# Kernel optimization log

Hardware: AMD Instinct MI355X
Metric: run time of the kernel (lower is better)

The kernel has to match this reference:

```python
import jax, jax.numpy as jnp
import numpy as np

H = 128  # hidden_dim
F = 64   # node_feat_dim


def setup_inputs() -> dict:
    key = jax.random.key(0)
    ks = jax.random.split(key, 24)
    N, E, NR, NT = 50000, 400000, 20000, 20000
    inp = {
        "mol_x": jax.random.normal(ks[0], (N, F), jnp.float32),
        "pos": jax.random.normal(ks[1], (N, 3), jnp.float32),
        "reaction_x": jax.random.normal(ks[2], (NR, F), jnp.float32),
        "target_x": jax.random.normal(ks[3], (NT, F), jnp.float32),
        "edge_index": jax.random.randint(ks[4], (2, E), 0, N, jnp.int32),
    }
    def lin(k, fan_in, fan_out):
        s = 1.0 / np.sqrt(fan_in)
        kw, kb = jax.random.split(k)
        W = jax.random.uniform(kw, (fan_in, fan_out), jnp.float32, -s, s)
        b = jax.random.uniform(kb, (fan_out,), jnp.float32, -s, s)
        return W, b
    inp["W_node"], inp["b_node"] = lin(ks[5], F, H)
    inp["W_att1"], inp["b_att1"] = lin(ks[6], 2 * H + 3, H)
    inp["W_att2"], inp["b_att2"] = lin(ks[7], H, 1)
    inp["W_upd"], inp["b_upd"] = lin(ks[8], H, H)
    inp["Wy1"], inp["by1"] = lin(ks[9], H, 64)
    inp["Wy2"], inp["by2"] = lin(ks[10], 64, 1)
    inp["Wa1"], inp["ba1"] = lin(ks[11], H, 64)
    inp["Wa2"], inp["ba2"] = lin(ks[12], 64, 1)
    return inp


def reference(mol_x, pos, reaction_x, target_x, edge_index,
              W_node, b_node, W_att1, b_att1, W_att2, b_att2,
              W_upd, b_upd, Wy1, by1, Wy2, by2, Wa1, ba1, Wa2, ba2):
    N = mol_x.shape[0]
    # node encoder
    h = mol_x @ W_node + b_node                      # [N, H]
    src, dst = edge_index[0], edge_index[1]          # PyG: x_j = source, x_i = target
    x_j = h[src]                                      # [E, H]
    x_i = h[dst]                                      # [E, H]
    dist = pos[dst] - pos[src]                        # [E, 3]
    cat = jnp.concatenate([x_i, x_j, dist], axis=1)   # [E, 2H+3]
    s = jax.nn.relu(cat @ W_att1 + b_att1) @ W_att2 + b_att2  # [E, 1]
    att = jax.nn.softmax(s, axis=0)                   # global softmax over edges (dim=0)
    msg = x_j * att                                   # [E, H]
    aggr = jax.ops.segment_sum(msg, dst, num_segments=N)  # scatter-add -> [N, H]
    mol_feats = aggr @ W_upd + b_upd                  # [N, H]
    # heads on reaction / target graphs
    rh = reaction_x @ W_node + b_node
    th = target_x @ W_node + b_node
    pred_yield = (jax.nn.relu(rh @ Wy1 + by1) @ Wy2 + by2).squeeze(-1)
    pred_activity = (jax.nn.relu(th @ Wa1 + ba1) @ Wa2 + ba2).squeeze(-1)
    return pred_yield, pred_activity, mol_feats
```

## Files before the change

### kernel.cpp

```cpp
#include <hip/hip_runtime.h>
#include <hip/hip_bf16.h>

typedef unsigned short ushort_t;
typedef __attribute__((ext_vector_type(8))) short s16x8;
typedef __attribute__((ext_vector_type(4))) float f32x4;

__device__ inline unsigned short f2bf(float x) {
    unsigned u = __float_as_uint(x);
    return (unsigned short)((u + 0x7FFFu + ((u >> 16) & 1u)) >> 16);
}
__device__ inline float bflo(unsigned u) { return __uint_as_float(u << 16); }
__device__ inline float bfhi(unsigned u) { return __uint_as_float(u & 0xffff0000u); }

__device__ inline void pack_one(const float* __restrict__ W, int K, int N,
                                ushort_t* __restrict__ dst, int g) {
    int KT = K / 32;
    int nt = g / (KT * 64);
    int rem = g % (KT * 64);
    int kt = rem / 64, lane = rem % 64;
    int n = nt * 16 + (lane & 15);
    int kbase = kt * 32 + ((lane >> 4) << 3);
    ushort_t tmp[8];
#pragma unroll
    for (int j = 0; j < 8; ++j) tmp[j] = f2bf(W[(size_t)(kbase + j) * N + n]);
    uint4 pk;
    pk.x = tmp[0] | ((unsigned)tmp[1] << 16);
    pk.y = tmp[2] | ((unsigned)tmp[3] << 16);
    pk.z = tmp[4] | ((unsigned)tmp[5] << 16);
    pk.w = tmp[6] | ((unsigned)tmp[7] << 16);
    *(uint4*)&dst[(size_t)g * 8] = pk;
}

__global__ void convert_w(const float* __restrict__ Wn, const float* __restrict__ W1,
                          const float* __restrict__ Wu, const float* __restrict__ Wy1,
                          const float* __restrict__ Wa1,
                          ushort_t* __restrict__ Wnb, ushort_t* __restrict__ W1tb,
                          ushort_t* __restrict__ W1mb, ushort_t* __restrict__ Wub,
                          ushort_t* __restrict__ Wy1b, ushort_t* __restrict__ Wa1b) {
    int t = blockIdx.x * 256 + threadIdx.x;
    if (t < 1024)       pack_one(Wn, 64, 128, Wnb, t);
    else if (t < 3072)  pack_one(W1, 128, 128, W1tb, t - 1024);
    else if (t < 5120)  pack_one(W1 + 128 * 128, 128, 128, W1mb, t - 3072);
    else if (t < 7168)  pack_one(Wu, 128, 128, Wub, t - 5120);
    else if (t < 8192)  pack_one(Wy1, 128, 64, Wy1b, t - 7168);
    else if (t < 9216)  pack_one(Wa1, 128, 64, Wa1b, t - 8192);
}

__global__ void encode_pq(const float* __restrict__ x, const ushort_t* __restrict__ Wnb,
                          const float* __restrict__ bn, const ushort_t* __restrict__ W1tb,
                          const ushort_t* __restrict__ W1mb, const float* __restrict__ b1,
                          ushort_t* __restrict__ hb, ushort_t* __restrict__ P,
                          ushort_t* __restrict__ Q, int nrows) {
    __shared__ ushort_t ldsX[16 * 72];
    __shared__ ushort_t ldsH[16 * 136];
    int t = threadIdx.x;
    int r0 = blockIdx.x * 16;
    {
        int row = t >> 4, c4 = (t & 15) * 4;
        float4 v = *(const float4*)&x[(size_t)(r0 + row) * 64 + c4];
        uint2 pk;
        pk.x = f2bf(v.x) | ((unsigned)f2bf(v.y) << 16);
        pk.y = f2bf(v.z) | ((unsigned)f2bf(v.w) << 16);
        *(uint2*)&ldsX[row * 72 + c4] = pk;
    }
    __syncthreads();
    int w = t >> 6, lane = t & 63;
    int c = lane & 15, q = lane >> 4;
    int ntA = w, ntB = w + 4;
    {
        f32x4 acc0 = {0.f, 0.f, 0.f, 0.f}, acc1 = acc0;
#pragma unroll
        for (int kt = 0; kt < 2; ++kt) {
            s16x8 a = *(const s16x8*)&ldsX[c * 72 + kt * 32 + q * 8];
            s16x8 b0 = *(const s16x8*)&Wnb[((ntA * 2 + kt) * 64 + lane) * 8];
            s16x8 b1v = *(const s16x8*)&Wnb[((ntB * 2 + kt) * 64 + lane) * 8];
            acc0 = __builtin_amdgcn_mfma_f32_16x16x32_bf16(a, b0, acc0, 0, 0, 0);
            acc1 = __builtin_amdgcn_mfma_f32_16x16x32_bf16(a, b1v, acc1, 0, 0, 0);
        }
        float bi0 = bn[ntA * 16 + c], bi1 = bn[ntB * 16 + c];
#pragma unroll
        for (int r = 0; r < 4; ++r) {
            int row = r0 + q * 4 + r;
            ushort_t h0 = f2bf(acc0[r] + bi0), h1 = f2bf(acc1[r] + bi1);
            ldsH[(q * 4 + r) * 136 + ntA * 16 + c] = h0;
            ldsH[(q * 4 + r) * 136 + ntB * 16 + c] = h1;
            if (row < nrows) {
                hb[(size_t)row * 128 + ntA * 16 + c] = h0;
                hb[(size_t)row * 128 + ntB * 16 + c] = h1;
            }
        }
    }
    __syncthreads();
    {
        f32x4 p0 = {0.f, 0.f, 0.f, 0.f}, p1 = p0, q0 = p0, q1 = p0;
#pragma unroll
        for (int kt = 0; kt < 4; ++kt) {
            s16x8 a = *(const s16x8*)&ldsH[c * 136 + kt * 32 + q * 8];
            s16x8 bp0 = *(const s16x8*)&W1tb[((ntA * 4 + kt) * 64 + lane) * 8];
            s16x8 bp1 = *(const s16x8*)&W1tb[((ntB * 4 + kt) * 64 + lane) * 8];
            s16x8 bq0 = *(const s16x8*)&W1mb[((ntA * 4 + kt) * 64 + lane) * 8];
            s16x8 bq1 = *(const s16x8*)&W1mb[((ntB * 4 + kt) * 64 + lane) * 8];
            p0 = __builtin_amdgcn_mfma_f32_16x16x32_bf16(a, bp0, p0, 0, 0, 0);
            p1 = __builtin_amdgcn_mfma_f32_16x16x32_bf16(a, bp1, p1, 0, 0, 0);
            q0 = __builtin_amdgcn_mfma_f32_16x16x32_bf16(a, bq0, q0, 0, 0, 0);
            q1 = __builtin_amdgcn_mfma_f32_16x16x32_bf16(a, bq1, q1, 0, 0, 0);
        }
        float bi0 = b1[ntA * 16 + c], bi1 = b1[ntB * 16 + c];
#pragma unroll
        for (int r = 0; r < 4; ++r) {
            int row = r0 + q * 4 + r;
            if (row < nrows) {
                P[(size_t)row * 128 + ntA * 16 + c] = f2bf(p0[r] + bi0);
                P[(size_t)row * 128 + ntB * 16 + c] = f2bf(p1[r] + bi1);
                Q[(size_t)row * 128 + ntA * 16 + c] = f2bf(q0[r]);
                Q[(size_t)row * 128 + ntB * 16 + c] = f2bf(q1[r]);
            }
        }
    }
}

__global__ void edge_score(const ushort_t* __restrict__ P, const ushort_t* __restrict__ Q,
                           const float* __restrict__ pos, const int* __restrict__ src,
                           const int* __restrict__ dst, const float* __restrict__ W1b,
                           const float* __restrict__ W2, const float* __restrict__ b2,
                           float* __restrict__ s_out, int* __restrict__ counts,
                           float* __restrict__ redm, float* __restrict__ rede, int E) {
    __shared__ float wsh[4 * 128];
    __shared__ float smm[256], sme[256];
    int t = threadIdx.x;
    for (int i = t; i < 384; i += 256) wsh[i] = W1b[i];
    if (t < 128) wsh[384 + t] = W2[t];
    __syncthreads();
    int w = t >> 6, lane = t & 63;
    int g = lane >> 4;
    int c = lane & 15;
    float w0[8], w1[8], w2[8], wv[8];
#pragma unroll
    for (int j = 0; j < 8; ++j) {
        w0[j] = wsh[c * 8 + j];
        w1[j] = wsh[128 + c * 8 + j];
        w2[j] = wsh[256 + c * 8 + j];
        wv[j] = wsh[384 + c * 8 + j];
    }
    float b2v = b2[0];
    int base = blockIdx.x * 64 + w * 16;
    float m = -1e30f, ev = 0.f;
#pragma unroll
    for (int it = 0; it < 4; ++it) {
        int e = base + it * 4 + g;
        bool valid = e < E;
        int ee = valid ? e : (E - 1);
        int sa = src[ee], da = dst[ee];
        uint4 pr = *(const uint4*)&P[(size_t)da * 128 + c * 8];
        uint4 qr = *(const uint4*)&Q[(size_t)sa * 128 + c * 8];
        float d0 = pos[da * 3]     - pos[sa * 3];
        float d1 = pos[da * 3 + 1] - pos[sa * 3 + 1];
        float d2 = pos[da * 3 + 2] - pos[sa * 3 + 2];
        unsigned pw[4] = {pr.x, pr.y, pr.z, pr.w};
        unsigned qw[4] = {qr.x, qr.y, qr.z, qr.w};
        float v = 0.f;
#pragma unroll
        for (int jj = 0; jj < 4; ++jj) {
            float pe = bflo(pw[jj]) + bflo(qw[jj])
                     + d0 * w0[2 * jj] + d1 * w1[2 * jj] + d2 * w2[2 * jj];
            float po = bfhi(pw[jj]) + bfhi(qw[jj])
                     + d0 * w0[2 * jj + 1] + d1 * w1[2 * jj + 1] + d2 * w2[2 * jj + 1];
            v += fmaxf(pe, 0.f) * wv[2 * jj] + fmaxf(po, 0.f) * wv[2 * jj + 1];
        }
#pragma unroll
        for (int off = 1; off < 16; off <<= 1) v += __shfl_xor(v, off, 64);
        float sv = v + b2v;
        if (c == 0 && valid) {
            s_out[e] = sv;
            atomicAdd(&counts[da], 1);
            float nm = fmaxf(m, sv);
            ev = ev * __expf(m - nm) + __expf(sv - nm);
            m = nm;
        }
    }
    smm[t] = m; sme[t] = ev; __syncthreads();
    for (int off = 128; off > 0; off >>= 1) {
        if (t < off) {
            float m1 = smm[t], m2 = smm[t + off];
            float e1 = sme[t], e2 = sme[t + off];
            float M = fmaxf(m1, m2);
            smm[t] = M;
            sme[t] = e1 * __expf(m1 - M) + e2 * __expf(m2 - M);
        }
        __syncthreads();
    }
    if (t == 0) { redm[blockIdx.x] = smm[0]; rede[blockIdx.x] = sme[0]; }
}

__global__ void smax2(const float* __restrict__ redm, const float* __restrict__ rede,
                      float* __restrict__ scal, int nb) {
    __shared__ float smm[256], sme[256];
    int t = threadIdx.x;
    float m = -1e30f, ev = 0.f;
    for (int i = t; i < nb; i += 256) {
        float m2 = redm[i], e2 = rede[i];
        float M = fmaxf(m, m2);
        ev = ev * __expf(m - M) + e2 * __expf(m2 - M);
        m = M;
    }
    smm[t] = m; sme[t] = ev; __syncthreads();
    for (int off = 128; off > 0; off >>= 1) {
        if (t < off) {
            float m1 = smm[t], m2 = smm[t + off];
            float e1 = sme[t], e2 = sme[t + off];
            float M = fmaxf(m1, m2);
            smm[t] = M;
            sme[t] = e1 * __expf(m1 - M) + e2 * __expf(m2 - M);
        }
        __syncthreads();
    }
    if (t == 0) { scal[0] = smm[0]; scal[1] = 1.f / sme[0]; }
}

__global__ void scan1(const int* __restrict__ counts, int* __restrict__ offs,
                      int* __restrict__ partials, int N) {
    __shared__ int sm[256];
    int i = blockIdx.x * 256 + threadIdx.x;
    int v = (i < N) ? counts[i] : 0;
    sm[threadIdx.x] = v; __syncthreads();
    for (int off = 1; off < 256; off <<= 1) {
        int add = (threadIdx.x >= off) ? sm[threadIdx.x - off] : 0;
        __syncthreads();
        sm[threadIdx.x] += add;
        __syncthreads();
    }
    if (i < N) offs[i] = sm[threadIdx.x] - v;
    if (threadIdx.x == 255) partials[blockIdx.x] = sm[255];
}

__global__ void scan2(int* __restrict__ partials, int nb) {
    __shared__ int sm[256];
    int v = (threadIdx.x < nb) ? partials[threadIdx.x] : 0;
    sm[threadIdx.x] = v; __syncthreads();
    for (int off = 1; off < 256; off <<= 1) {
        int add = (threadIdx.x >= off) ? sm[threadIdx.x - off] : 0;
        __syncthreads();
        sm[threadIdx.x] += add;
        __syncthreads();
    }
    if (threadIdx.x < nb) partials[threadIdx.x] = sm[threadIdx.x] - v;
}

__global__ void scan3(int* __restrict__ offs, int* __restrict__ cursor,
                      const int* __restrict__ partials, int N) {
    int i = blockIdx.x * 256 + threadIdx.x;
    if (i < N) {
        int v = offs[i] + partials[blockIdx.x];
        offs[i] = v;
        cursor[i] = v;
    }
}

__global__ void fill_csr(const int* __restrict__ src, const int* __restrict__ dst,
                         int* __restrict__ cursor, int2* __restrict__ csr, int E) {
    int e = blockIdx.x * 256 + threadIdx.x;
    if (e >= E) return;
    int p = atomicAdd(&cursor[dst[e]], 1);
    csr[p] = make_int2(e, src[e]);
}

__global__ void gather_upd(const ushort_t* __restrict__ hb, const int2* __restrict__ csr,
                           const int* __restrict__ offs, const int* __restrict__ deg,
                           const float* __restrict__ s, const float* __restrict__ scal,
                           const ushort_t* __restrict__ Wub, const float* __restrict__ bu,
                           float* __restrict__ C, int N) {
    __shared__ ushort_t ldsA[16 * 136];
    int t = threadIdx.x;
    int w = t >> 6, lane = t & 63;
    int half = lane >> 5, l32 = lane & 31;
    int r0 = blockIdx.x * 16;
    float m = scal[0], inv = scal[1];
#pragma unroll
    for (int i = 0; i < 4; ++i) {
        int node = r0 + w * 4 + i;
        float a0 = 0.f, a1 = 0.f, a2 = 0.f, a3 = 0.f;
        if (node < N) {
            int start = offs[node], d = deg[node];
            for (int k = half; k < d; k += 2) {
                int2 es = csr[start + k];
                float att = __expf(s[es.x] - m) * inv;
                uint2 hq = *(const uint2*)&hb[(size_t)es.y * 128 + l32 * 4];
                a0 += bflo(hq.x) * att;
                a1 += bfhi(hq.x) * att;
                a2 += bflo(hq.y) * att;
                a3 += bfhi(hq.y) * att;
            }
        }
        a0 += __shfl_xor(a0, 32, 64);
        a1 += __shfl_xor(a1, 32, 64);
        a2 += __shfl_xor(a2, 32, 64);
        a3 += __shfl_xor(a3, 32, 64);
        if (half == 0) {
            uint2 pk;
            pk.x = f2bf(a0) | ((unsigned)f2bf(a1) << 16);
            pk.y = f2bf(a2) | ((unsigned)f2bf(a3) << 16);
            *(uint2*)&ldsA[(w * 4 + i) * 136 + l32 * 4] = pk;
        }
    }
    __syncthreads();
    int c = lane & 15, q = lane >> 4;
    int ntA = w, ntB = w + 4;
    f32x4 acc0 = {0.f, 0.f, 0.f, 0.f}, acc1 = acc0;
#pragma unroll
    for (int kt = 0; kt < 4; ++kt) {
        s16x8 a = *(const s16x8*)&ldsA[c * 136 + kt * 32 + q * 8];
        s16x8 b0 = *(const s16x8*)&Wub[((ntA * 4 + kt) * 64 + lane) * 8];
        s16x8 b1 = *(const s16x8*)&Wub[((ntB * 4 + kt) * 64 + lane) * 8];
        acc0 = __builtin_amdgcn_mfma_f32_16x16x32_bf16(a, b0, acc0, 0, 0, 0);
        acc1 = __builtin_amdgcn_mfma_f32_16x16x32_bf16(a, b1, acc1, 0, 0, 0);
    }
    float bi0 = bu[ntA * 16 + c], bi1 = bu[ntB * 16 + c];
#pragma unroll
    for (int r = 0; r < 4; ++r) {
        int row = r0 + q * 4 + r;
        if (row < N) {
            C[(size_t)row * 128 + ntA * 16 + c] = acc0[r] + bi0;
            C[(size_t)row * 128 + ntB * 16 + c] = acc1[r] + bi1;
        }
    }
}

__global__ void head_mfma(const float* __restrict__ rx, const float* __restrict__ tx,
                          const ushort_t* __restrict__ Wnb, const float* __restrict__ bn,
                          const ushort_t* __restrict__ Wy1b, const float* __restrict__ by1,
                          const float* __restrict__ Wy2, const float* __restrict__ by2,
                          const ushort_t* __restrict__ Wa1b, const float* __restrict__ ba1,
                          const float* __restrict__ Wa2, const float* __restrict__ ba2,
                          float* __restrict__ out, int nb1, int NR, int NT) {
    __shared__ ushort_t ldsA[16 * 72];
    __shared__ ushort_t ldsB[16 * 136];
    __shared__ float part[64];
    int blk = blockIdx.x;
    const float* x; const ushort_t* W1b; const float* b1; const float* W2; const float* b2;
    float* o; int r0, nrows;
    if (blk < nb1) { x = rx; W1b = Wy1b; b1 = by1; W2 = Wy2; b2 = by2; o = out; r0 = blk * 16; nrows = NR; }
    else { x = tx; W1b = Wa1b; b1 = ba1; W2 = Wa2; b2 = ba2; o = out + NR; r0 = (blk - nb1) * 16; nrows = NT; }

    int t = threadIdx.x;
    {
        int row = t >> 4, c4 = (t & 15) * 4;
        float4 v = *(const float4*)&x[(size_t)(r0 + row) * 64 + c4];
        uint2 pk;
        pk.x = f2bf(v.x) | ((unsigned)f2bf(v.y) << 16);
        pk.y = f2bf(v.z) | ((unsigned)f2bf(v.w) << 16);
        *(uint2*)&ldsA[row * 72 + c4] = pk;
    }
    __syncthreads();
    int w = t >> 6, lane = t & 63;
    int c = lane & 15, q = lane >> 4;
    {
        int ntA = w, ntB = w + 4;
        f32x4 acc0 = {0.f, 0.f, 0.f, 0.f}, acc1 = acc0;
#pragma unroll
        for (int kt = 0; kt < 2; ++kt) {
            s16x8 a = *(const s16x8*)&ldsA[c * 72 + kt * 32 + q * 8];
            s16x8 b0 = *(const s16x8*)&Wnb[((ntA * 2 + kt) * 64 + lane) * 8];
            s16x8 b1v = *(const s16x8*)&Wnb[((ntB * 2 + kt) * 64 + lane) * 8];
            acc0 = __builtin_amdgcn_mfma_f32_16x16x32_bf16(a, b0, acc0, 0, 0, 0);
            acc1 = __builtin_amdgcn_mfma_f32_16x16x32_bf16(a, b1v, acc1, 0, 0, 0);
        }
        float bi0 = bn[ntA * 16 + c], bi1 = bn[ntB * 16 + c];
#pragma unroll
        for (int r = 0; r < 4; ++r) {
            int row = q * 4 + r;
            ldsB[row * 136 + ntA * 16 + c] = f2bf(acc0[r] + bi0);
            ldsB[row * 136 + ntB * 16 + c] = f2bf(acc1[r] + bi1);
        }
    }
    __syncthreads();
    {
        f32x4 acc = {0.f, 0.f, 0.f, 0.f};
#pragma unroll
        for (int kt = 0; kt < 4; ++kt) {
            s16x8 a = *(const s16x8*)&ldsB[c * 136 + kt * 32 + q * 8];
            s16x8 b0 = *(const s16x8*)&W1b[((w * 4 + kt) * 64 + lane) * 8];
            acc = __builtin_amdgcn_mfma_f32_16x16x32_bf16(a, b0, acc, 0, 0, 0);
        }
        float bi = b1[w * 16 + c], w2v = W2[w * 16 + c];
#pragma unroll
        for (int r = 0; r < 4; ++r) {
            float u = fmaxf(acc[r] + bi, 0.f) * w2v;
#pragma unroll
            for (int mm = 1; mm < 16; mm <<= 1) u += __shfl_xor(u, mm, 64);
            if (c == 0) part[w * 16 + q * 4 + r] = u;
        }
    }
    __syncthreads();
    if (t < 16) {
        int row = r0 + t;
        if (row < nrows)
            o[row] = part[t] + part[16 + t] + part[32 + t] + part[48 + t] + b2[0];
    }
}

extern "C" void kernel_launch(void* const* d_in, const int* in_sizes, int n_in,
                              void* d_out, int out_size, void* d_ws, size_t ws_size,
                              hipStream_t stream) {
    const float* mol_x      = (const float*)d_in[0];
    const float* pos        = (const float*)d_in[1];
    const float* reaction_x = (const float*)d_in[2];
    const float* target_x   = (const float*)d_in[3];
    const int*   ei         = (const int*)d_in[4];
    const float* W_node = (const float*)d_in[5];
    const float* b_node = (const float*)d_in[6];
    const float* W_att1 = (const float*)d_in[7];
    const float* b_att1 = (const float*)d_in[8];
    const float* W_att2 = (const float*)d_in[9];
    const float* b_att2 = (const float*)d_in[10];
    const float* W_upd  = (const float*)d_in[11];
    const float* b_upd  = (const float*)d_in[12];
    const float* Wy1 = (const float*)d_in[13];
    const float* by1 = (const float*)d_in[14];
    const float* Wy2 = (const float*)d_in[15];
    const float* by2 = (const float*)d_in[16];
    const float* Wa1 = (const float*)d_in[17];
    const float* ba1 = (const float*)d_in[18];
    const float* Wa2 = (const float*)d_in[19];
    const float* ba2 = (const float*)d_in[20];

    int N  = in_sizes[0] / 64;
    int E  = in_sizes[4] / 2;
    int NR = in_sizes[2] / 64;
    int NT = in_sizes[3] / 64;

    float* out = (float*)d_out;

    int nbE = (E + 63) / 64;

    char* wp = (char*)d_ws;
    ushort_t* hb = (ushort_t*)wp;  wp += (size_t)N * 128 * 2;
    ushort_t* Qb = (ushort_t*)wp;  wp += (size_t)N * 128 * 2;
    float* s     = (float*)wp;     wp += (size_t)E * 4;
    float* redm  = (float*)wp;     wp += (size_t)nbE * 4;
    float* rede  = (float*)wp;     wp += (size_t)nbE * 4;
    float* scal  = (float*)wp;     wp += 4 * 4;
    int* counts  = (int*)wp;       wp += (size_t)N * 4;
    int* offs    = (int*)wp;       wp += (size_t)N * 4;
    int* cursor  = (int*)wp;       wp += (size_t)N * 4;
    int* partials= (int*)wp;       wp += 256 * 4;
    int2* csr    = (int2*)wp;      wp += (size_t)E * 8;
    ushort_t* Wnb  = (ushort_t*)wp; wp += 8192 * 2;
    ushort_t* W1tb = (ushort_t*)wp; wp += 16384 * 2;
    ushort_t* W1mb = (ushort_t*)wp; wp += 16384 * 2;
    ushort_t* Wub  = (ushort_t*)wp; wp += 16384 * 2;
    ushort_t* Wy1b = (ushort_t*)wp; wp += 8192 * 2;
    ushort_t* Wa1b = (ushort_t*)wp; wp += 8192 * 2;
    ushort_t* Pb = (ushort_t*)(out + NR + NT);
    float* molf  = out + NR + NT;

    const int* srcp = ei;
    const int* dstp = ei + E;
    int nbN = (N + 255) / 256;

    hipMemsetAsync(counts, 0, (size_t)N * sizeof(int), stream);
    convert_w<<<36, 256, 0, stream>>>(W_node, W_att1, W_upd, Wy1, Wa1,
                                      Wnb, W1tb, W1mb, Wub, Wy1b, Wa1b);
    encode_pq<<<(N + 15) / 16, 256, 0, stream>>>(mol_x, Wnb, b_node, W1tb, W1mb, b_att1,
                                                 hb, Pb, Qb, N);
    edge_score<<<nbE, 256, 0, stream>>>(Pb, Qb, pos, srcp, dstp,
                                        W_att1 + 256 * 128, W_att2, b_att2,
                                        s, counts, redm, rede, E);
    smax2<<<1, 256, 0, stream>>>(redm, rede, scal, nbE);
    scan1<<<nbN, 256, 0, stream>>>(counts, offs, partials, N);
    scan2<<<1, 256, 0, stream>>>(partials, nbN);
    scan3<<<nbN, 256, 0, stream>>>(offs, cursor, partials, N);
    fill_csr<<<(E + 255) / 256, 256, 0, stream>>>(srcp, dstp, cursor, csr, E);
    gather_upd<<<(N + 15) / 16, 256, 0, stream>>>(hb, csr, offs, counts, s, scal,
                                                  Wub, b_upd, molf, N);
    head_mfma<<<(NR + NT) / 16, 256, 0, stream>>>(reaction_x, target_x, Wnb, b_node,
                                                  Wy1b, by1, Wy2, by2, Wa1b, ba1, Wa2, ba2,
                                                  out, NR / 16, NR, NT);
}
```

Before: 256.3 us.

## Fuse memset and scan stages, restructure encode, batch edge loads, widen gather

Folds the counts memset into the weight-conversion kernel and merges the two scan fixup kernels into one that recomputes the block prefix itself, which cuts launches. encode_pq now gives each wave its own 16 rows, so one block covers 64 rows, and the A operand is loaded straight into registers. edge_score issues all index and row loads before the compute loop to raise memory-level parallelism. fill_csr stores the edge score inside the CSR entry, so the gather avoids an indirect lookup, and gather_upd reads 16-byte rows with four edges in flight per node. The cost is more register pressure and extra shuffles in the reduction.

```diff
diff --git a/kernel.cpp b/kernel.cpp
--- a/kernel.cpp
+++ b/kernel.cpp
@@ -36,7 +36,8 @@
                           const float* __restrict__ Wa1,
                           ushort_t* __restrict__ Wnb, ushort_t* __restrict__ W1tb,
                           ushort_t* __restrict__ W1mb, ushort_t* __restrict__ Wub,
-                          ushort_t* __restrict__ Wy1b, ushort_t* __restrict__ Wa1b) {
+                          ushort_t* __restrict__ Wy1b, ushort_t* __restrict__ Wa1b,
+                          int* __restrict__ counts, int N) {
     int t = blockIdx.x * 256 + threadIdx.x;
     if (t < 1024)       pack_one(Wn, 64, 128, Wnb, t);
     else if (t < 3072)  pack_one(W1, 128, 128, W1tb, t - 1024);
@@ -44,6 +45,7 @@
     else if (t < 7168)  pack_one(Wu, 128, 128, Wub, t - 5120);
     else if (t < 8192)  pack_one(Wy1, 128, 64, Wy1b, t - 7168);
     else if (t < 9216)  pack_one(Wa1, 128, 64, Wa1b, t - 8192);
+    if (t < N) counts[t] = 0;
 }
 
 __global__ void encode_pq(const float* __restrict__ x, const ushort_t* __restrict__ Wnb,
@@ -51,69 +53,66 @@
                           const ushort_t* __restrict__ W1mb, const float* __restrict__ b1,
                           ushort_t* __restrict__ hb, ushort_t* __restrict__ P,
                           ushort_t* __restrict__ Q, int nrows) {
-    __shared__ ushort_t ldsX[16 * 72];
-    __shared__ ushort_t ldsH[16 * 136];
-    int t = threadIdx.x;
-    int r0 = blockIdx.x * 16;
-    {
-        int row = t >> 4, c4 = (t & 15) * 4;
-        float4 v = *(const float4*)&x[(size_t)(r0 + row) * 64 + c4];
-        uint2 pk;
-        pk.x = f2bf(v.x) | ((unsigned)f2bf(v.y) << 16);
-        pk.y = f2bf(v.z) | ((unsigned)f2bf(v.w) << 16);
-        *(uint2*)&ldsX[row * 72 + c4] = pk;
-    }
-    __syncthreads();
+    __shared__ ushort_t ldsH[4 * 16 * 136];
+    int t = threadIdx.x;
     int w = t >> 6, lane = t & 63;
     int c = lane & 15, q = lane >> 4;
-    int ntA = w, ntB = w + 4;
-    {
-        f32x4 acc0 = {0.f, 0.f, 0.f, 0.f}, acc1 = acc0;
+    int r0 = blockIdx.x * 64 + w * 16;
+    int rowA = r0 + c; if (rowA >= nrows) rowA = nrows - 1;
+    ushort_t* myH = &ldsH[w * 16 * 136];
+
+    s16x8 xa[2];
+#pragma unroll
+    for (int kt = 0; kt < 2; ++kt) {
+        const float* xp = &x[(size_t)rowA * 64 + kt * 32 + q * 8];
+        float4 v0 = *(const float4*)xp;
+        float4 v1 = *(const float4*)(xp + 4);
+        s16x8 a;
+        a[0] = (short)f2bf(v0.x); a[1] = (short)f2bf(v0.y);
+        a[2] = (short)f2bf(v0.z); a[3] = (short)f2bf(v0.w);
+        a[4] = (short)f2bf(v1.x); a[5] = (short)f2bf(v1.y);
+        a[6] = (short)f2bf(v1.z); a[7] = (short)f2bf(v1.w);
+        xa[kt] = a;
+    }
+#pragma unroll
+    for (int nt = 0; nt < 8; ++nt) {
+        f32x4 acc = {0.f, 0.f, 0.f, 0.f};
 #pragma unroll
         for (int kt = 0; kt < 2; ++kt) {
-            s16x8 a = *(const s16x8*)&ldsX[c * 72 + kt * 32 + q * 8];
-            s16x8 b0 = *(const s16x8*)&Wnb[((ntA * 2 + kt) * 64 + lane) * 8];
-            s16x8 b1v = *(const s16x8*)&Wnb[((ntB * 2 + kt) * 64 + lane) * 8];
-            acc0 = __builtin_amdgcn_mfma_f32_16x16x32_bf16(a, b0, acc0, 0, 0, 0);
-            acc1 = __builtin_amdgcn_mfma_f32_16x16x32_bf16(a, b1v, acc1, 0, 0, 0);
-        }
-        float bi0 = bn[ntA * 16 + c], bi1 = bn[ntB * 16 + c];
+            s16x8 b = *(const s16x8*)&Wnb[((nt * 2 + kt) * 64 + lane) * 8];
+            acc = __builtin_amdgcn_mfma_f32_16x16x32_bf16(xa[kt], b, acc, 0, 0, 0);
+        }
+        float bi = bn[nt * 16 + c];
 #pragma unroll
         for (int r = 0; r < 4; ++r) {
             int row = r0 + q * 4 + r;
-            ushort_t h0 = f2bf(acc0[r] + bi0), h1 = f2bf(acc1[r] + bi1);
-            ldsH[(q * 4 + r) * 136 + ntA * 16 + c] = h0;
-            ldsH[(q * 4 + r) * 136 + ntB * 16 + c] = h1;
-            if (row < nrows) {
-                hb[(size_t)row * 128 + ntA * 16 + c] = h0;
-                hb[(size_t)row * 128 + ntB * 16 + c] = h1;
-            }
-        }
-    }
-    __syncthreads();
-    {
-        f32x4 p0 = {0.f, 0.f, 0.f, 0.f}, p1 = p0, q0 = p0, q1 = p0;
+            ushort_t hv = f2bf(acc[r] + bi);
+            myH[(q * 4 + r) * 136 + nt * 16 + c] = hv;
+            if (row < nrows) hb[(size_t)row * 128 + nt * 16 + c] = hv;
+        }
+    }
+    __syncthreads();
+    s16x8 ha[4];
+#pragma unroll
+    for (int kt = 0; kt < 4; ++kt)
+        ha[kt] = *(const s16x8*)&myH[c * 136 + kt * 32 + q * 8];
+#pragma unroll
+    for (int nt = 0; nt < 8; ++nt) {
+        f32x4 pa = {0.f, 0.f, 0.f, 0.f}, qa = pa;
 #pragma unroll
         for (int kt = 0; kt < 4; ++kt) {
-            s16x8 a = *(const s16x8*)&ldsH[c * 136 + kt * 32 + q * 8];
-            s16x8 bp0 = *(const s16x8*)&W1tb[((ntA * 4 + kt) * 64 + lane) * 8];
-            s16x8 bp1 = *(const s16x8*)&W1tb[((ntB * 4 + kt) * 64 + lane) * 8];
-            s16x8 bq0 = *(const s16x8*)&W1mb[((ntA * 4 + kt) * 64 + lane) * 8];
-            s16x8 bq1 = *(const s16x8*)&W1mb[((ntB * 4 + kt) * 64 + lane) * 8];
-            p0 = __builtin_amdgcn_mfma_f32_16x16x32_bf16(a, bp0, p0, 0, 0, 0);
-            p1 = __builtin_amdgcn_mfma_f32_16x16x32_bf16(a, bp1, p1, 0, 0, 0);
-            q0 = __builtin_amdgcn_mfma_f32_16x16x32_bf16(a, bq0, q0, 0, 0, 0);
-            q1 = __builtin_amdgcn_mfma_f32_16x16x32_bf16(a, bq1, q1, 0, 0, 0);
-        }
-        float bi0 = b1[ntA * 16 + c], bi1 = b1[ntB * 16 + c];
+            s16x8 bp = *(const s16x8*)&W1tb[((nt * 4 + kt) * 64 + lane) * 8];
+            s16x8 bq = *(const s16x8*)&W1mb[((nt * 4 + kt) * 64 + lane) * 8];
+            pa = __builtin_amdgcn_mfma_f32_16x16x32_bf16(ha[kt], bp, pa, 0, 0, 0);
+            qa = __builtin_amdgcn_mfma_f32_16x16x32_bf16(ha[kt], bq, qa, 0, 0, 0);
+        }
+        float bi = b1[nt * 16 + c];
 #pragma unroll
         for (int r = 0; r < 4; ++r) {
             int row = r0 + q * 4 + r;
             if (row < nrows) {
-                P[(size_t)row * 128 + ntA * 16 + c] = f2bf(p0[r] + bi0);
-                P[(size_t)row * 128 + ntB * 16 + c] = f2bf(p1[r] + bi1);
-                Q[(size_t)row * 128 + ntA * 16 + c] = f2bf(q0[r]);
-                Q[(size_t)row * 128 + ntB * 16 + c] = f2bf(q1[r]);
+                P[(size_t)row * 128 + nt * 16 + c] = f2bf(pa[r] + bi);
+                Q[(size_t)row * 128 + nt * 16 + c] = f2bf(qa[r]);
             }
         }
     }
@@ -132,8 +131,7 @@
     if (t < 128) wsh[384 + t] = W2[t];
     __syncthreads();
     int w = t >> 6, lane = t & 63;
-    int g = lane >> 4;
-    int c = lane & 15;
+    int g = lane >> 4, c = lane & 15;
     float w0[8], w1[8], w2[8], wv[8];
 #pragma unroll
     for (int j = 0; j < 8; ++j) {
@@ -145,19 +143,31 @@
     float b2v = b2[0];
     int base = blockIdx.x * 64 + w * 16;
     float m = -1e30f, ev = 0.f;
+
+    int sa[4], da[4];
+#pragma unroll
+    for (int it = 0; it < 4; ++it) {
+        int e = base + it * 4 + g;
+        int ee = (e < E) ? e : (E - 1);
+        sa[it] = src[ee]; da[it] = dst[ee];
+    }
+    uint4 pr[4], qr[4];
+    float dd0[4], dd1[4], dd2[4];
+#pragma unroll
+    for (int it = 0; it < 4; ++it) {
+        pr[it] = *(const uint4*)&P[(size_t)da[it] * 128 + c * 8];
+        qr[it] = *(const uint4*)&Q[(size_t)sa[it] * 128 + c * 8];
+        dd0[it] = pos[da[it] * 3]     - pos[sa[it] * 3];
+        dd1[it] = pos[da[it] * 3 + 1] - pos[sa[it] * 3 + 1];
+        dd2[it] = pos[da[it] * 3 + 2] - pos[sa[it] * 3 + 2];
+    }
 #pragma unroll
     for (int it = 0; it < 4; ++it) {
         int e = base + it * 4 + g;
         bool valid = e < E;
-        int ee = valid ? e : (E - 1);
-        int sa = src[ee], da = dst[ee];
-        uint4 pr = *(const uint4*)&P[(size_t)da * 128 + c * 8];
-        uint4 qr = *(const uint4*)&Q[(size_t)sa * 128 + c * 8];
-        float d0 = pos[da * 3]     - pos[sa * 3];
-        float d1 = pos[da * 3 + 1] - pos[sa * 3 + 1];
-        float d2 = pos[da * 3 + 2] - pos[sa * 3 + 2];
-        unsigned pw[4] = {pr.x, pr.y, pr.z, pr.w};
-        unsigned qw[4] = {qr.x, qr.y, qr.z, qr.w};
+        unsigned pw[4] = {pr[it].x, pr[it].y, pr[it].z, pr[it].w};
+        unsigned qw[4] = {qr[it].x, qr[it].y, qr[it].z, qr[it].w};
+        float d0 = dd0[it], d1 = dd1[it], d2 = dd2[it];
         float v = 0.f;
 #pragma unroll
         for (int jj = 0; jj < 4; ++jj) {
@@ -172,7 +182,7 @@
         float sv = v + b2v;
         if (c == 0 && valid) {
             s_out[e] = sv;
-            atomicAdd(&counts[da], 1);
+            atomicAdd(&counts[da[it]], 1);
             float nm = fmaxf(m, sv);
             ev = ev * __expf(m - nm) + __expf(sv - nm);
             m = nm;
@@ -233,86 +243,86 @@
     if (threadIdx.x == 255) partials[blockIdx.x] = sm[255];
 }
 
-__global__ void scan2(int* __restrict__ partials, int nb) {
+__global__ void scan_add(int* __restrict__ offs, int* __restrict__ cursor,
+                         const int* __restrict__ partials, int nb, int N) {
     __shared__ int sm[256];
-    int v = (threadIdx.x < nb) ? partials[threadIdx.x] : 0;
-    sm[threadIdx.x] = v; __syncthreads();
-    for (int off = 1; off < 256; off <<= 1) {
-        int add = (threadIdx.x >= off) ? sm[threadIdx.x - off] : 0;
+    int t = threadIdx.x;
+    sm[t] = (t < nb && t < blockIdx.x) ? partials[t] : 0;
+    __syncthreads();
+    for (int off = 128; off > 0; off >>= 1) {
+        if (t < off) sm[t] += sm[t + off];
         __syncthreads();
-        sm[threadIdx.x] += add;
-        __syncthreads();
-    }
-    if (threadIdx.x < nb) partials[threadIdx.x] = sm[threadIdx.x] - v;
-}
-
-__global__ void scan3(int* __restrict__ offs, int* __restrict__ cursor,
-                      const int* __restrict__ partials, int N) {
-    int i = blockIdx.x * 256 + threadIdx.x;
+    }
+    int basev = sm[0];
+    int i = blockIdx.x * 256 + t;
     if (i < N) {
-        int v = offs[i] + partials[blockIdx.x];
+        int v = offs[i] + basev;
         offs[i] = v;
         cursor[i] = v;
     }
 }
 
 __global__ void fill_csr(const int* __restrict__ src, const int* __restrict__ dst,
-                         int* __restrict__ cursor, int2* __restrict__ csr, int E) {
+                         const float* __restrict__ s, int* __restrict__ cursor,
+                         int2* __restrict__ csr, int E) {
     int e = blockIdx.x * 256 + threadIdx.x;
     if (e >= E) return;
     int p = atomicAdd(&cursor[dst[e]], 1);
-    csr[p] = make_int2(e, src[e]);
+    csr[p] = make_int2(src[e], __float_as_int(s[e]));
 }
 
 __global__ void gather_upd(const ushort_t* __restrict__ hb, const int2* __restrict__ csr,
                            const int* __restrict__ offs, const int* __restrict__ deg,
-                           const float* __restrict__ s, const float* __restrict__ scal,
+                           const float* __restrict__ scal,
                            const ushort_t* __restrict__ Wub, const float* __restrict__ bu,
                            float* __restrict__ C, int N) {
     __shared__ ushort_t ldsA[16 * 136];
     int t = threadIdx.x;
     int w = t >> 6, lane = t & 63;
-    int half = lane >> 5, l32 = lane & 31;
+    int g = lane >> 4, c = lane & 15;
     int r0 = blockIdx.x * 16;
     float m = scal[0], inv = scal[1];
 #pragma unroll
     for (int i = 0; i < 4; ++i) {
         int node = r0 + w * 4 + i;
-        float a0 = 0.f, a1 = 0.f, a2 = 0.f, a3 = 0.f;
+        float a[8] = {0.f, 0.f, 0.f, 0.f, 0.f, 0.f, 0.f, 0.f};
         if (node < N) {
             int start = offs[node], d = deg[node];
-            for (int k = half; k < d; k += 2) {
-                int2 es = csr[start + k];
-                float att = __expf(s[es.x] - m) * inv;
-                uint2 hq = *(const uint2*)&hb[(size_t)es.y * 128 + l32 * 4];
-                a0 += bflo(hq.x) * att;
-                a1 += bfhi(hq.x) * att;
-                a2 += bflo(hq.y) * att;
-                a3 += bfhi(hq.y) * att;
+            for (int k = g; k < d; k += 4) {
+                int2 v = csr[start + k];
+                float att = __expf(__int_as_float(v.y) - m) * inv;
+                uint4 hq = *(const uint4*)&hb[(size_t)v.x * 128 + c * 8];
+                a[0] += bflo(hq.x) * att; a[1] += bfhi(hq.x) * att;
+                a[2] += bflo(hq.y) * att; a[3] += bfhi(hq.y) * att;
+                a[4] += bflo(hq.z) * att; a[5] += bfhi(hq.z) * att;
+                a[6] += bflo(hq.w) * att; a[7] += bfhi(hq.w) * att;
             }
         }
-        a0 += __shfl_xor(a0, 32, 64);
-        a1 += __shfl_xor(a1, 32, 64);
-        a2 += __shfl_xor(a2, 32, 64);
-        a3 += __shfl_xor(a3, 32, 64);
-        if (half == 0) {
-            uint2 pk;
-            pk.x = f2bf(a0) | ((unsigned)f2bf(a1) << 16);
-            pk.y = f2bf(a2) | ((unsigned)f2bf(a3) << 16);
-            *(uint2*)&ldsA[(w * 4 + i) * 136 + l32 * 4] = pk;
-        }
-    }
-    __syncthreads();
-    int c = lane & 15, q = lane >> 4;
+#pragma unroll
+        for (int j = 0; j < 8; ++j) {
+            a[j] += __shfl_xor(a[j], 16, 64);
+            a[j] += __shfl_xor(a[j], 32, 64);
+        }
+        if (g == 0) {
+            uint4 pk;
+            pk.x = f2bf(a[0]) | ((unsigned)f2bf(a[1]) << 16);
+            pk.y = f2bf(a[2]) | ((unsigned)f2bf(a[3]) << 16);
+            pk.z = f2bf(a[4]) | ((unsigned)f2bf(a[5]) << 16);
+            pk.w = f2bf(a[6]) | ((unsigned)f2bf(a[7]) << 16);
+            *(uint4*)&ldsA[(w * 4 + i) * 136 + c * 8] = pk;
+        }
+    }
+    __syncthreads();
+    int q = lane >> 4;
     int ntA = w, ntB = w + 4;
     f32x4 acc0 = {0.f, 0.f, 0.f, 0.f}, acc1 = acc0;
 #pragma unroll
     for (int kt = 0; kt < 4; ++kt) {
-        s16x8 a = *(const s16x8*)&ldsA[c * 136 + kt * 32 + q * 8];
+        s16x8 av = *(const s16x8*)&ldsA[c * 136 + kt * 32 + q * 8];
         s16x8 b0 = *(const s16x8*)&Wub[((ntA * 4 + kt) * 64 + lane) * 8];
         s16x8 b1 = *(const s16x8*)&Wub[((ntB * 4 + kt) * 64 + lane) * 8];
-        acc0 = __builtin_amdgcn_mfma_f32_16x16x32_bf16(a, b0, acc0, 0, 0, 0);
-        acc1 = __builtin_amdgcn_mfma_f32_16x16x32_bf16(a, b1, acc1, 0, 0, 0);
+        acc0 = __builtin_amdgcn_mfma_f32_16x16x32_bf16(av, b0, acc0, 0, 0, 0);
+        acc1 = __builtin_amdgcn_mfma_f32_16x16x32_bf16(av, b1, acc1, 0, 0, 0);
     }
     float bi0 = bu[ntA * 16 + c], bi1 = bu[ntB * 16 + c];
 #pragma unroll
@@ -457,20 +467,18 @@
     const int* dstp = ei + E;
     int nbN = (N + 255) / 256;
 
-    hipMemsetAsync(counts, 0, (size_t)N * sizeof(int), stream);
-    convert_w<<<36, 256, 0, stream>>>(W_node, W_att1, W_upd, Wy1, Wa1,
-                                      Wnb, W1tb, W1mb, Wub, Wy1b, Wa1b);
-    encode_pq<<<(N + 15) / 16, 256, 0, stream>>>(mol_x, Wnb, b_node, W1tb, W1mb, b_att1,
+    convert_w<<<nbN, 256, 0, stream>>>(W_node, W_att1, W_upd, Wy1, Wa1,
+                                       Wnb, W1tb, W1mb, Wub, Wy1b, Wa1b, counts, N);
+    encode_pq<<<(N + 63) / 64, 256, 0, stream>>>(mol_x, Wnb, b_node, W1tb, W1mb, b_att1,
                                                  hb, Pb, Qb, N);
     edge_score<<<nbE, 256, 0, stream>>>(Pb, Qb, pos, srcp, dstp,
                                         W_att1 + 256 * 128, W_att2, b_att2,
                                         s, counts, redm, rede, E);
     smax2<<<1, 256, 0, stream>>>(redm, rede, scal, nbE);
     scan1<<<nbN, 256, 0, stream>>>(counts, offs, partials, N);
-    scan2<<<1, 256, 0, stream>>>(partials, nbN);
-    scan3<<<nbN, 256, 0, stream>>>(offs, cursor, partials, N);
-    fill_csr<<<(E + 255) / 256, 256, 0, stream>>>(srcp, dstp, cursor, csr, E);
-    gather_upd<<<(N + 15) / 16, 256, 0, stream>>>(hb, csr, offs, counts, s, scal,
+    scan_add<<<nbN, 256, 0, stream>>>(offs, cursor, partials, nbN, N);
+    fill_csr<<<(E + 255) / 256, 256, 0, stream>>>(srcp, dstp, s, cursor, csr, E);
+    gather_upd<<<(N + 15) / 16, 256, 0, stream>>>(hb, csr, offs, counts, scal,
                                                   Wub, b_upd, molf, N);
     head_mfma<<<(NR + NT) / 16, 256, 0, stream>>>(reaction_x, target_x, Wnb, b_node,
                                                   Wy1b, by1, Wy2, by2, Wa1b, ba1, Wa2, ba2,
```

Measured after the change: 249.3 us. -2.7%, faster.
